# Optimization experiments

Hardware: AMD Instinct MI355X
Metric: run time of the kernel (lower is better)

The kernel has to match this reference:

```python
import jax, jax.numpy as jnp
import numpy as np

DROP_P = 0.5
DROP_KEY = jax.random.key(42)  # fixed key: deterministic dropout mask


def setup_inputs() -> dict:
    key = jax.random.key(0)
    k1, k2, k3 = jax.random.split(key, 3)
    B, H, S, D = 2, 16, 2048, 128
    x1 = jax.random.normal(k1, (B, H, S, D), dtype=jnp.float32)
    x2 = jax.random.normal(k2, (B, H, S, D), dtype=jnp.float32)
    # broadcastable per-head divisor; offset to keep it away from zero
    x3 = jax.random.uniform(k3, (B, H, 1, 1), dtype=jnp.float32) + 1.0
    return {"x1": x1, "x2": x2, "x3": x3}


def reference(x1, x2, x3):
    # v1 = x1 @ x2^T  -> [B,H,S,S]; v2 = v1 / x3 (broadcast divisor)
    scores = jnp.einsum('bhqd,bhkd->bhqk', x1, x2) / x3
    # v3 = softmax over last dim
    probs = jax.nn.softmax(scores, axis=-1)
    # v4 = dropout(p=0.5), training=True semantics: mask and rescale by 1/(1-p)
    keep = jax.random.bernoulli(DROP_KEY, 1.0 - DROP_P, probs.shape)
    probs = jnp.where(keep, probs / (1.0 - DROP_P), 0.0)
    # v5 = v4 @ x1 (note: values are x1, not a separate V); v6 = v5 + x2 residual
    out = jnp.einsum('bhqk,bhkd->bhqd', probs, x1) + x2
    return out
```

## Files before the change

kernel.cpp:

```cpp
#include <hip/hip_runtime.h>
#include <math.h>


constexpr int Sc = 2048, Dc = 128;
constexpr int NT = 32;
constexpr int BUF = 32768;
constexpr int VREL = 16384;
constexpr int POFF = 65536;

typedef short bf16x8 __attribute__((ext_vector_type(8)));
typedef float f32x4 __attribute__((ext_vector_type(4)));
union U8 { uint4 u; bf16x8 v; };

__device__ __forceinline__ unsigned rotl(unsigned x, int r) {
  return __builtin_amdgcn_alignbit(x, x, 32 - r);
}

__device__ __forceinline__ unsigned tf_o0(unsigned x1) {
  const unsigned ks1 = 42u;
  const unsigned ks2 = 0x1BD11BDAu ^ 42u;
  unsigned x0 = 0u; x1 += ks1;
#define TFR(r) { x0 += x1; x1 = rotl(x1, r); x1 ^= x0; }
  TFR(13) TFR(15) TFR(26) TFR(6)
  x0 += ks1; x1 += ks2 + 1u;
  TFR(17) TFR(29) TFR(16) TFR(24)
  x0 += ks2; x1 += 0u + 2u;
  TFR(13) TFR(15) TFR(26) TFR(6)
  x1 += ks1 + 3u;
  TFR(17) TFR(29) TFR(16) TFR(24)
  x0 += ks1; x1 += ks2 + 4u;
  TFR(13) TFR(15) TFR(26)
  x0 += x1;
  x0 += ks2;
#undef TFR
  return x0;
}

__device__ __forceinline__ unsigned keepmask(unsigned idx) {
  return (unsigned)(((int)~tf_o0(idx)) >> 31);
}

__device__ __forceinline__ unsigned pk2rn(float a, float b) {
  return __builtin_amdgcn_perm(__float_as_uint(b) + 0x8000u,
                               __float_as_uint(a) + 0x8000u, 0x07060302u);
}

__device__ __forceinline__ unsigned hw2(unsigned ma, unsigned mb) {
  return __builtin_amdgcn_perm(mb, ma, 0x05040100u);
}

__device__ __forceinline__ void gload16(const void* g, void* l) {
  __builtin_amdgcn_global_load_lds(
      (const __attribute__((address_space(1))) void*)g,
      (__attribute__((address_space(3))) void*)l, 16, 0, 0);
}

__device__ __forceinline__ void masks8(unsigned ib, unsigned km[8]) {
#pragma unroll
  for (int h2 = 0; h2 < 4; ++h2) {
    unsigned a0 = keepmask(ib + h2 * 16 + 0), a1 = keepmask(ib + h2 * 16 + 1);
    unsigned a2 = keepmask(ib + h2 * 16 + 2), a3 = keepmask(ib + h2 * 16 + 3);
    km[h2 * 2 + 0] = hw2(a0, a1);
    km[h2 * 2 + 1] = hw2(a2, a3);
  }
}

__global__ __launch_bounds__(256)
void prepack(const float* __restrict__ x1, const float* __restrict__ x2,
             uint4* __restrict__ Kb, uint4* __restrict__ Vt) {
  __shared__ ushort Kl[32 * 136];
  __shared__ ushort Vl[32 * 136];
  const int tid = threadIdx.x;
  const size_t tile = blockIdx.x;
  const float4* ks = (const float4*)(x2 + tile * 4096);
  const float4* vs = (const float4*)(x1 + tile * 4096);
#pragma unroll
  for (int it = 0; it < 4; ++it) {
    int f = it * 256 + tid;
    int row = f >> 5, c4 = f & 31;
    float4 kv = ks[f];
    float4 vv = vs[f];
    *(uint2*)&Kl[row * 136 + c4 * 4] = uint2{pk2rn(kv.x, kv.y), pk2rn(kv.z, kv.w)};
    *(uint2*)&Vl[row * 136 + c4 * 4] = uint2{pk2rn(vv.x, vv.y), pk2rn(vv.z, vv.w)};
  }
  __syncthreads();
#pragma unroll
  for (int it = 0; it < 2; ++it) {
    int u = it * 256 + tid;
    int lane = u & 63, grp = u >> 6;
    int mt = grp >> 2, c = grp & 3, m16 = lane & 15, g = lane >> 4;
    Kb[tile * 512 + u] = *(const uint4*)&Kl[(mt * 16 + m16) * 136 + c * 32 + g * 8];
  }
#pragma unroll
  for (int it = 0; it < 2; ++it) {
    int u = it * 256 + tid;
    int lane = u & 63, dt = u >> 6, m16 = lane & 15, g = lane >> 4;
    int d = dt * 16 + m16, k0 = g * 8;
    unsigned w[4];
#pragma unroll
    for (int p = 0; p < 4; ++p) {
      unsigned lo = Vl[(k0 + 2 * p) * 136 + d];
      unsigned hi = Vl[(k0 + 2 * p + 1) * 136 + d];
      w[p] = lo | (hi << 16);
    }
    Vt[tile * 512 + u] = uint4{w[0], w[1], w[2], w[3]};
  }
}

__global__ __launch_bounds__(256, 2)
void attn7(const uint4* __restrict__ Kb, const uint4* __restrict__ Vt,
           const float* __restrict__ x1, const float* __restrict__ x2,
           const float* __restrict__ x3, float* __restrict__ out) {
  __shared__ uint4 smemv[(POFF + 8192) / 16];
  char* smem = (char*)smemv;
  float* Os = (float*)smem;

  const int tid = threadIdx.x, wave = tid >> 6, lane = tid & 63;
  const int g = lane >> 4, q = lane & 15;
  const int blk = blockIdx.x, bh = blk & 31, qt = blk >> 5;

  const float* X1 = x1 + (size_t)bh * (Sc * Dc);
  const float* X2 = x2 + (size_t)bh * (Sc * Dc);
  float* outp = out + (size_t)bh * (Sc * Dc);
  const float cl2 = (1.0f / x3[bh]) * 1.4426950408889634f;

  const int qrow = qt * 64 + wave * 16 + q;
  const unsigned row_base = (unsigned)(bh * Sc + qrow) * (unsigned)Sc;
  char* prow = smem + POFF + wave * 2048 + q * 128;

  const size_t tg = (size_t)bh * 64;
  const int off = wave * 1024 + lane * 16;

  auto issue = [&](int tt, int bb) {
    const char* kg = (const char*)(Kb + (tg + 2 * tt) * 512);
    const char* vg = (const char*)(Vt + (tg + 2 * tt) * 512);
#pragma unroll
    for (int h = 0; h < 2; ++h) {
      gload16(kg + h * 8192 + off,        smem + bb + h * 8192 + off);
      gload16(kg + h * 8192 + off + 4096, smem + bb + h * 8192 + off + 4096);
      gload16(vg + h * 8192 + off,        smem + bb + VREL + h * 8192 + off);
      gload16(vg + h * 8192 + off + 4096, smem + bb + VREL + h * 8192 + off + 4096);
    }
  };

  bf16x8 qf[4];
  {
    const float4* qsrc = (const float4*)(X1 + (size_t)qrow * Dc);
#pragma unroll
    for (int c = 0; c < 4; ++c) {
      float4 f0 = qsrc[c * 8 + g * 2], f1 = qsrc[c * 8 + g * 2 + 1];
      U8 cv; cv.u = uint4{pk2rn(f0.x, f0.y), pk2rn(f0.z, f0.w),
                          pk2rn(f1.x, f1.y), pk2rn(f1.z, f1.w)};
      qf[c] = cv.v;
    }
  }

  f32x4 o[8];
#pragma unroll
  for (int i = 0; i < 8; ++i) o[i] = f32x4{0.f, 0.f, 0.f, 0.f};
  float l_run = 0.0f;

  issue(0, 0);
  __builtin_amdgcn_sched_barrier(0);
  unsigned kmc[8], kmn[8];
  masks8(row_base + (unsigned)(g * 4), kmc);

  for (int t = 0; t < NT; ++t) {
    __syncthreads();

    if (t < NT - 1) issue(t + 1, ((t + 1) & 1) * BUF);
    __builtin_amdgcn_sched_barrier(0);

    const char* kb = smem + (t & 1) * BUF;
    const char* vb = kb + VREL;

    f32x4 s0 = {}, s1 = {}, s2 = {}, s3 = {};
#pragma unroll
    for (int c = 0; c < 4; ++c) {
      U8 a0; a0.u = *(const uint4*)(kb +        ((0 * 4 + c) * 64 + lane) * 16);
      U8 a1; a1.u = *(const uint4*)(kb +        ((1 * 4 + c) * 64 + lane) * 16);
      U8 a2; a2.u = *(const uint4*)(kb + 8192 + ((0 * 4 + c) * 64 + lane) * 16);
      U8 a3; a3.u = *(const uint4*)(kb + 8192 + ((1 * 4 + c) * 64 + lane) * 16);
      s0 = __builtin_amdgcn_mfma_f32_16x16x32_bf16(a0.v, qf[c], s0, 0, 0, 0);
      s1 = __builtin_amdgcn_mfma_f32_16x16x32_bf16(a1.v, qf[c], s1, 0, 0, 0);
      s2 = __builtin_amdgcn_mfma_f32_16x16x32_bf16(a2.v, qf[c], s2, 0, 0, 0);
      s3 = __builtin_amdgcn_mfma_f32_16x16x32_bf16(a3.v, qf[c], s3, 0, 0, 0);
    }

    if (t < NT - 1)
      masks8(row_base + (unsigned)((t + 1) * 64) + (unsigned)(g * 4), kmn);

    float pr[16];
    float ls = 0.0f;
#pragma unroll
    for (int i = 0; i < 4; ++i) { pr[i]      = __builtin_amdgcn_exp2f(s0[i] * cl2); ls += pr[i]; }
#pragma unroll
    for (int i = 0; i < 4; ++i) { pr[4 + i]  = __builtin_amdgcn_exp2f(s1[i] * cl2); ls += pr[4 + i]; }
#pragma unroll
    for (int i = 0; i < 4; ++i) { pr[8 + i]  = __builtin_amdgcn_exp2f(s2[i] * cl2); ls += pr[8 + i]; }
#pragma unroll
    for (int i = 0; i < 4; ++i) { pr[12 + i] = __builtin_amdgcn_exp2f(s3[i] * cl2); ls += pr[12 + i]; }
    ls += __shfl_xor(ls, 16);
    ls += __shfl_xor(ls, 32);
    l_run += ls;

#pragma unroll
    for (int h2 = 0; h2 < 4; ++h2) {
      unsigned w0 = pk2rn(pr[h2 * 4 + 0], pr[h2 * 4 + 1]) & kmc[h2 * 2 + 0];
      unsigned w1 = pk2rn(pr[h2 * 4 + 2], pr[h2 * 4 + 3]) & kmc[h2 * 2 + 1];
      int u = (h2 >> 1) * 8 + (h2 & 1) * 4 + g;
      *(uint2*)(prow + ((u ^ q) & 15) * 8) = uint2{w0, w1};
    }

    U8 bf0, bf1;
    {
      int u0 = 2 * g;
      uint2 lo0 = *(const uint2*)(prow + (((u0 + 0) ^ q) & 15) * 8);
      uint2 hi0 = *(const uint2*)(prow + (((u0 + 1) ^ q) & 15) * 8);
      bf0.u = uint4{lo0.x, lo0.y, hi0.x, hi0.y};
      int u1 = 8 + 2 * g;
      uint2 lo1 = *(const uint2*)(prow + (((u1 + 0) ^ q) & 15) * 8);
      uint2 hi1 = *(const uint2*)(prow + (((u1 + 1) ^ q) & 15) * 8);
      bf1.u = uint4{lo1.x, lo1.y, hi1.x, hi1.y};
    }

#pragma unroll
    for (int dt = 0; dt < 8; ++dt) {
      U8 av0; av0.u = *(const uint4*)(vb +        (dt * 64 + lane) * 16);
      U8 av1; av1.u = *(const uint4*)(vb + 8192 + (dt * 64 + lane) * 16);
      o[dt] = __builtin_amdgcn_mfma_f32_16x16x32_bf16(av0.v, bf0.v, o[dt], 0, 0, 0);
      o[dt] = __builtin_amdgcn_mfma_f32_16x16x32_bf16(av1.v, bf1.v, o[dt], 0, 0, 0);
    }

#pragma unroll
    for (int i = 0; i < 8; ++i) kmc[i] = kmn[i];
  }

  const float invl = 2.0f / l_run;
  __syncthreads();
  {
    float* ow = Os + (size_t)(wave * 16 + q) * 132;
#pragma unroll
    for (int dt = 0; dt < 8; ++dt) {
      int d = dt * 16 + g * 4;
      *(float4*)&ow[d] = float4{o[dt][0] * invl, o[dt][1] * invl,
                                o[dt][2] * invl, o[dt][3] * invl};
    }
  }
  __syncthreads();
#pragma unroll
  for (int it = 0; it < 8; ++it) {
    int f = it * 256 + tid;
    int ql = f >> 5, c4 = f & 31;
    float4 ov = *(const float4*)&Os[ql * 132 + c4 * 4];
    size_t goff = (size_t)(qt * 64 + ql) * Dc + c4 * 4;
    float4 xv = *(const float4*)&X2[goff];
    *(float4*)&outp[goff] = float4{ov.x + xv.x, ov.y + xv.y, ov.z + xv.z, ov.w + xv.w};
  }
}

extern "C" void kernel_launch(void* const* d_in, const int* in_sizes, int n_in,
                              void* d_out, int out_size, void* d_ws, size_t ws_size,
                              hipStream_t stream) {
  const float* x1 = (const float*)d_in[0];
  const float* x2 = (const float*)d_in[1];
  const float* x3 = (const float*)d_in[2];
  float* out = (float*)d_out;
  const size_t PREP = (size_t)2048 * 512 * 16;
  uint4* Kb = (uint4*)d_ws;
  uint4* Vtg = (uint4*)((char*)d_ws + PREP);
  prepack<<<2048, 256, 0, stream>>>(x1, x2, Kb, Vtg);
  attn7<<<1024, 256, 0, stream>>>(Kb, Vtg, x1, x2, x3, out);
}
```

Measured before the change: 402.5 us.

## Precompute dropout keep-mask bits in prepack and stream them into attention

The Threefry-based dropout mask is now computed once per element in the prepack kernel and packed as 16-bit words in the workspace, laid out in the attention kernel's per-thread access order. The attention kernel then loads one 16-bit mask word per tile per thread, prefetched one tile ahead, instead of hashing 16 indices inline. This takes the integer hash work out of the MFMA/exp loop. In exchange, prepack does all the hashing serially per thread and writes a 16 MB mask buffer that attention must read back.

Result: no change. 410.2 us (+1.9%).

```diff
diff --git a/kernel.cpp b/kernel.cpp
--- a/kernel.cpp
+++ b/kernel.cpp
@@ -36,8 +36,8 @@
   return x0;
 }
 
-__device__ __forceinline__ unsigned keepmask(unsigned idx) {
-  return (unsigned)(((int)~tf_o0(idx)) >> 31);
+__device__ __forceinline__ unsigned kb(unsigned mw, int pos) {
+  return (unsigned)(((int)(mw << (31 - pos))) >> 31);
 }
 
 __device__ __forceinline__ unsigned pk2rn(float a, float b) {
@@ -55,21 +55,13 @@
       (__attribute__((address_space(3))) void*)l, 16, 0, 0);
 }
 
-__device__ __forceinline__ void masks8(unsigned ib, unsigned km[8]) {
-#pragma unroll
-  for (int h2 = 0; h2 < 4; ++h2) {
-    unsigned a0 = keepmask(ib + h2 * 16 + 0), a1 = keepmask(ib + h2 * 16 + 1);
-    unsigned a2 = keepmask(ib + h2 * 16 + 2), a3 = keepmask(ib + h2 * 16 + 3);
-    km[h2 * 2 + 0] = hw2(a0, a1);
-    km[h2 * 2 + 1] = hw2(a2, a3);
-  }
-}
-
 __global__ __launch_bounds__(256)
 void prepack(const float* __restrict__ x1, const float* __restrict__ x2,
-             uint4* __restrict__ Kb, uint4* __restrict__ Vt) {
+             uint4* __restrict__ Kb, uint4* __restrict__ Vt,
+             unsigned* __restrict__ Mw) {
   __shared__ ushort Kl[32 * 136];
   __shared__ ushort Vl[32 * 136];
+  __shared__ ushort Ml[32 * 128];
   const int tid = threadIdx.x;
   const size_t tile = blockIdx.x;
   const float4* ks = (const float4*)(x2 + tile * 4096);
@@ -83,7 +75,31 @@
     *(uint2*)&Kl[row * 136 + c4 * 4] = uint2{pk2rn(kv.x, kv.y), pk2rn(kv.z, kv.w)};
     *(uint2*)&Vl[row * 136 + c4 * 4] = uint2{pk2rn(vv.x, vv.y), pk2rn(vv.z, vv.w)};
   }
+
+  {
+    const unsigned a    = (unsigned)tile * 128u + (unsigned)(tid >> 1);
+    const unsigned th   = (unsigned)(tid & 1);
+    const unsigned ablk = a >> 8, atid = a & 255u;
+    const unsigned bh = ablk & 31u, qt = ablk >> 5;
+    const unsigned wv = atid >> 6, ln = atid & 63u;
+    const unsigned g = ln >> 4, q = ln & 15u;
+    const unsigned row = bh * 2048u + qt * 64u + wv * 16u + q;
+    const unsigned fb = row * 2048u + g * 4u + th * 1024u;
+    const int atid2 = tid >> 1;
+    for (int tt = 0; tt < 16; ++tt) {
+      unsigned w = 0;
+#pragma unroll
+      for (int h2 = 0; h2 < 4; ++h2)
+#pragma unroll
+        for (int i = 0; i < 4; ++i) {
+          unsigned o0 = tf_o0(fb + (unsigned)(tt * 64 + h2 * 16 + i));
+          w |= (o0 >> 31) << (h2 * 4 + i);
+        }
+      Ml[(th * 16 + tt) * 128 + atid2] = (ushort)(~w & 0xFFFFu);
+    }
+  }
   __syncthreads();
+
 #pragma unroll
   for (int it = 0; it < 2; ++it) {
     int u = it * 256 + tid;
@@ -105,10 +121,22 @@
     }
     Vt[tile * 512 + u] = uint4{w[0], w[1], w[2], w[3]};
   }
+
+  {
+    const unsigned ablk = (unsigned)(tile >> 1), h = (unsigned)(tile & 1);
+    const unsigned* Mu = (const unsigned*)Ml;
+#pragma unroll
+    for (int k = 0; k < 8; ++k) {
+      int L = tid + k * 256;
+      int t = L >> 6, j2 = L & 63;
+      Mw[ablk * 4096u + (unsigned)t * 128u + h * 64u + (unsigned)j2] = Mu[L];
+    }
+  }
 }
 
 __global__ __launch_bounds__(256, 2)
-void attn7(const uint4* __restrict__ Kb, const uint4* __restrict__ Vt,
+void attn8(const uint4* __restrict__ Kb, const uint4* __restrict__ Vt,
+           const ushort* __restrict__ Mwu,
            const float* __restrict__ x1, const float* __restrict__ x2,
            const float* __restrict__ x3, float* __restrict__ out) {
   __shared__ uint4 smemv[(POFF + 8192) / 16];
@@ -125,11 +153,11 @@
   const float cl2 = (1.0f / x3[bh]) * 1.4426950408889634f;
 
   const int qrow = qt * 64 + wave * 16 + q;
-  const unsigned row_base = (unsigned)(bh * Sc + qrow) * (unsigned)Sc;
   char* prow = smem + POFF + wave * 2048 + q * 128;
 
   const size_t tg = (size_t)bh * 64;
   const int off = wave * 1024 + lane * 16;
+  const unsigned mbase = (unsigned)blk * 8192u + (unsigned)tid;
 
   auto issue = [&](int tt, int bb) {
     const char* kg = (const char*)(Kb + (tg + 2 * tt) * 512);
@@ -162,34 +190,34 @@
 
   issue(0, 0);
   __builtin_amdgcn_sched_barrier(0);
-  unsigned kmc[8], kmn[8];
-  masks8(row_base + (unsigned)(g * 4), kmc);
+  unsigned mwc = Mwu[mbase];
+  unsigned mwn = 0;
 
   for (int t = 0; t < NT; ++t) {
     __syncthreads();
 
-    if (t < NT - 1) issue(t + 1, ((t + 1) & 1) * BUF);
+    if (t < NT - 1) {
+      issue(t + 1, ((t + 1) & 1) * BUF);
+      mwn = Mwu[mbase + (unsigned)(t + 1) * 256u];
+    }
     __builtin_amdgcn_sched_barrier(0);
 
-    const char* kb = smem + (t & 1) * BUF;
-    const char* vb = kb + VREL;
+    const char* kb_ = smem + (t & 1) * BUF;
+    const char* vb = kb_ + VREL;
 
     f32x4 s0 = {}, s1 = {}, s2 = {}, s3 = {};
 #pragma unroll
     for (int c = 0; c < 4; ++c) {
-      U8 a0; a0.u = *(const uint4*)(kb +        ((0 * 4 + c) * 64 + lane) * 16);
-      U8 a1; a1.u = *(const uint4*)(kb +        ((1 * 4 + c) * 64 + lane) * 16);
-      U8 a2; a2.u = *(const uint4*)(kb + 8192 + ((0 * 4 + c) * 64 + lane) * 16);
-      U8 a3; a3.u = *(const uint4*)(kb + 8192 + ((1 * 4 + c) * 64 + lane) * 16);
+      U8 a0; a0.u = *(const uint4*)(kb_ +        ((0 * 4 + c) * 64 + lane) * 16);
+      U8 a1; a1.u = *(const uint4*)(kb_ +        ((1 * 4 + c) * 64 + lane) * 16);
+      U8 a2; a2.u = *(const uint4*)(kb_ + 8192 + ((0 * 4 + c) * 64 + lane) * 16);
+      U8 a3; a3.u = *(const uint4*)(kb_ + 8192 + ((1 * 4 + c) * 64 + lane) * 16);
       s0 = __builtin_amdgcn_mfma_f32_16x16x32_bf16(a0.v, qf[c], s0, 0, 0, 0);
       s1 = __builtin_amdgcn_mfma_f32_16x16x32_bf16(a1.v, qf[c], s1, 0, 0, 0);
       s2 = __builtin_amdgcn_mfma_f32_16x16x32_bf16(a2.v, qf[c], s2, 0, 0, 0);
       s3 = __builtin_amdgcn_mfma_f32_16x16x32_bf16(a3.v, qf[c], s3, 0, 0, 0);
     }
 
-    if (t < NT - 1)
-      masks8(row_base + (unsigned)((t + 1) * 64) + (unsigned)(g * 4), kmn);
-
     float pr[16];
     float ls = 0.0f;
 #pragma unroll
@@ -206,8 +234,10 @@
 
 #pragma unroll
     for (int h2 = 0; h2 < 4; ++h2) {
-      unsigned w0 = pk2rn(pr[h2 * 4 + 0], pr[h2 * 4 + 1]) & kmc[h2 * 2 + 0];
-      unsigned w1 = pk2rn(pr[h2 * 4 + 2], pr[h2 * 4 + 3]) & kmc[h2 * 2 + 1];
+      unsigned m0 = hw2(kb(mwc, h2 * 4 + 0), kb(mwc, h2 * 4 + 1));
+      unsigned m1 = hw2(kb(mwc, h2 * 4 + 2), kb(mwc, h2 * 4 + 3));
+      unsigned w0 = pk2rn(pr[h2 * 4 + 0], pr[h2 * 4 + 1]) & m0;
+      unsigned w1 = pk2rn(pr[h2 * 4 + 2], pr[h2 * 4 + 3]) & m1;
       int u = (h2 >> 1) * 8 + (h2 & 1) * 4 + g;
       *(uint2*)(prow + ((u ^ q) & 15) * 8) = uint2{w0, w1};
     }
@@ -232,8 +262,7 @@
       o[dt] = __builtin_amdgcn_mfma_f32_16x16x32_bf16(av1.v, bf1.v, o[dt], 0, 0, 0);
     }
 
-#pragma unroll
-    for (int i = 0; i < 8; ++i) kmc[i] = kmn[i];
+    mwc = mwn;
   }
 
   const float invl = 2.0f / l_run;
@@ -269,6 +298,7 @@
   const size_t PREP = (size_t)2048 * 512 * 16;
   uint4* Kb = (uint4*)d_ws;
   uint4* Vtg = (uint4*)((char*)d_ws + PREP);
-  prepack<<<2048, 256, 0, stream>>>(x1, x2, Kb, Vtg);
-  attn7<<<1024, 256, 0, stream>>>(Kb, Vtg, x1, x2, x3, out);
-}
+  unsigned* Mw = (unsigned*)((char*)d_ws + 2 * PREP);
+  prepack<<<2048, 256, 0, stream>>>(x1, x2, Kb, Vtg, Mw);
+  attn8<<<1024, 256, 0, stream>>>(Kb, Vtg, (const ushort*)Mw, x1, x2, x3, out);
+}
```

## Load K/V tiles directly from global into registers, drop LDS double buffering

Applied to the files above, without the earlier changes.

Replaces the async global-to-LDS double-buffered K/V staging with per-wave direct global loads into registers, since each wave reads the full K/V tile anyway (served from L2). LDS usage shrinks to the small P-transpose scratch and launch bounds rise to 8 blocks per SM for more occupancy. The epilogue now writes output directly from registers instead of staging through LDS. It risks exposed global-load latency without explicit prefetch, redundant L2 traffic across the four waves, and register pressure limiting the intended occupancy.

Result: slower. 892.2 us (+121.7%).

```diff
diff --git a/kernel.cpp b/kernel.cpp
--- a/kernel.cpp
+++ b/kernel.cpp
@@ -4,9 +4,6 @@
 
 constexpr int Sc = 2048, Dc = 128;
 constexpr int NT = 32;
-constexpr int BUF = 32768;
-constexpr int VREL = 16384;
-constexpr int POFF = 65536;
 
 typedef short bf16x8 __attribute__((ext_vector_type(8)));
 typedef float f32x4 __attribute__((ext_vector_type(4)));
@@ -49,12 +46,6 @@
   return __builtin_amdgcn_perm(mb, ma, 0x05040100u);
 }
 
-__device__ __forceinline__ void gload16(const void* g, void* l) {
-  __builtin_amdgcn_global_load_lds(
-      (const __attribute__((address_space(1))) void*)g,
-      (__attribute__((address_space(3))) void*)l, 16, 0, 0);
-}
-
 __device__ __forceinline__ void masks8(unsigned ib, unsigned km[8]) {
 #pragma unroll
   for (int h2 = 0; h2 < 4; ++h2) {
@@ -107,13 +98,12 @@
   }
 }
 
-__global__ __launch_bounds__(256, 2)
-void attn7(const uint4* __restrict__ Kb, const uint4* __restrict__ Vt,
-           const float* __restrict__ x1, const float* __restrict__ x2,
-           const float* __restrict__ x3, float* __restrict__ out) {
-  __shared__ uint4 smemv[(POFF + 8192) / 16];
+__global__ __launch_bounds__(256, 8)
+void attn11(const uint4* __restrict__ Kb, const uint4* __restrict__ Vt,
+            const float* __restrict__ x1, const float* __restrict__ x2,
+            const float* __restrict__ x3, float* __restrict__ out) {
+  __shared__ uint4 smemv[8192 / 16];
   char* smem = (char*)smemv;
-  float* Os = (float*)smem;
 
   const int tid = threadIdx.x, wave = tid >> 6, lane = tid & 63;
   const int g = lane >> 4, q = lane & 15;
@@ -126,22 +116,9 @@
 
   const int qrow = qt * 64 + wave * 16 + q;
   const unsigned row_base = (unsigned)(bh * Sc + qrow) * (unsigned)Sc;
-  char* prow = smem + POFF + wave * 2048 + q * 128;
+  char* prow = smem + wave * 2048 + q * 128;
 
   const size_t tg = (size_t)bh * 64;
-  const int off = wave * 1024 + lane * 16;
-
-  auto issue = [&](int tt, int bb) {
-    const char* kg = (const char*)(Kb + (tg + 2 * tt) * 512);
-    const char* vg = (const char*)(Vt + (tg + 2 * tt) * 512);
-#pragma unroll
-    for (int h = 0; h < 2; ++h) {
-      gload16(kg + h * 8192 + off,        smem + bb + h * 8192 + off);
-      gload16(kg + h * 8192 + off + 4096, smem + bb + h * 8192 + off + 4096);
-      gload16(vg + h * 8192 + off,        smem + bb + VREL + h * 8192 + off);
-      gload16(vg + h * 8192 + off + 4096, smem + bb + VREL + h * 8192 + off + 4096);
-    }
-  };
 
   bf16x8 qf[4];
   {
@@ -160,35 +137,34 @@
   for (int i = 0; i < 8; ++i) o[i] = f32x4{0.f, 0.f, 0.f, 0.f};
   float l_run = 0.0f;
 
-  issue(0, 0);
-  __builtin_amdgcn_sched_barrier(0);
-  unsigned kmc[8], kmn[8];
-  masks8(row_base + (unsigned)(g * 4), kmc);
-
   for (int t = 0; t < NT; ++t) {
-    __syncthreads();
-
-    if (t < NT - 1) issue(t + 1, ((t + 1) & 1) * BUF);
-    __builtin_amdgcn_sched_barrier(0);
-
-    const char* kb = smem + (t & 1) * BUF;
-    const char* vb = kb + VREL;
+    const uint4* Kg = Kb + (tg + 2 * (size_t)t) * 512;
+    const uint4* Vg = Vt + (tg + 2 * (size_t)t) * 512;
+
+    U8 kf[16];
+#pragma unroll
+    for (int mc = 0; mc < 8; ++mc) kf[mc].u      = Kg[mc * 64 + lane];
+#pragma unroll
+    for (int mc = 0; mc < 8; ++mc) kf[8 + mc].u  = Kg[512 + mc * 64 + lane];
+
+    unsigned km[8];
+    masks8(row_base + (unsigned)(t * 64) + (unsigned)(g * 4), km);
 
     f32x4 s0 = {}, s1 = {}, s2 = {}, s3 = {};
 #pragma unroll
     for (int c = 0; c < 4; ++c) {
-      U8 a0; a0.u = *(const uint4*)(kb +        ((0 * 4 + c) * 64 + lane) * 16);
-      U8 a1; a1.u = *(const uint4*)(kb +        ((1 * 4 + c) * 64 + lane) * 16);
-      U8 a2; a2.u = *(const uint4*)(kb + 8192 + ((0 * 4 + c) * 64 + lane) * 16);
-      U8 a3; a3.u = *(const uint4*)(kb + 8192 + ((1 * 4 + c) * 64 + lane) * 16);
-      s0 = __builtin_amdgcn_mfma_f32_16x16x32_bf16(a0.v, qf[c], s0, 0, 0, 0);
-      s1 = __builtin_amdgcn_mfma_f32_16x16x32_bf16(a1.v, qf[c], s1, 0, 0, 0);
-      s2 = __builtin_amdgcn_mfma_f32_16x16x32_bf16(a2.v, qf[c], s2, 0, 0, 0);
-      s3 = __builtin_amdgcn_mfma_f32_16x16x32_bf16(a3.v, qf[c], s3, 0, 0, 0);
-    }
-
-    if (t < NT - 1)
-      masks8(row_base + (unsigned)((t + 1) * 64) + (unsigned)(g * 4), kmn);
+      s0 = __builtin_amdgcn_mfma_f32_16x16x32_bf16(kf[c].v,      qf[c], s0, 0, 0, 0);
+      s1 = __builtin_amdgcn_mfma_f32_16x16x32_bf16(kf[4 + c].v,  qf[c], s1, 0, 0, 0);
+      s2 = __builtin_amdgcn_mfma_f32_16x16x32_bf16(kf[8 + c].v,  qf[c], s2, 0, 0, 0);
+      s3 = __builtin_amdgcn_mfma_f32_16x16x32_bf16(kf[12 + c].v, qf[c], s3, 0, 0, 0);
+    }
+
+    U8 vf0[8], vf1[8];
+#pragma unroll
+    for (int dt = 0; dt < 8; ++dt) {
+      vf0[dt].u = Vg[dt * 64 + lane];
+      vf1[dt].u = Vg[512 + dt * 64 + lane];
+    }
 
     float pr[16];
     float ls = 0.0f;
@@ -206,8 +182,8 @@
 
 #pragma unroll
     for (int h2 = 0; h2 < 4; ++h2) {
-      unsigned w0 = pk2rn(pr[h2 * 4 + 0], pr[h2 * 4 + 1]) & kmc[h2 * 2 + 0];
-      unsigned w1 = pk2rn(pr[h2 * 4 + 2], pr[h2 * 4 + 3]) & kmc[h2 * 2 + 1];
+      unsigned w0 = pk2rn(pr[h2 * 4 + 0], pr[h2 * 4 + 1]) & km[h2 * 2 + 0];
+      unsigned w1 = pk2rn(pr[h2 * 4 + 2], pr[h2 * 4 + 3]) & km[h2 * 2 + 1];
       int u = (h2 >> 1) * 8 + (h2 & 1) * 4 + g;
       *(uint2*)(prow + ((u ^ q) & 15) * 8) = uint2{w0, w1};
     }
@@ -226,36 +202,20 @@
 
 #pragma unroll
     for (int dt = 0; dt < 8; ++dt) {
-      U8 av0; av0.u = *(const uint4*)(vb +        (dt * 64 + lane) * 16);
-      U8 av1; av1.u = *(const uint4*)(vb + 8192 + (dt * 64 + lane) * 16);
-      o[dt] = __builtin_amdgcn_mfma_f32_16x16x32_bf16(av0.v, bf0.v, o[dt], 0, 0, 0);
-      o[dt] = __builtin_amdgcn_mfma_f32_16x16x32_bf16(av1.v, bf1.v, o[dt], 0, 0, 0);
-    }
-
-#pragma unroll
-    for (int i = 0; i < 8; ++i) kmc[i] = kmn[i];
+      o[dt] = __builtin_amdgcn_mfma_f32_16x16x32_bf16(vf0[dt].v, bf0.v, o[dt], 0, 0, 0);
+      o[dt] = __builtin_amdgcn_mfma_f32_16x16x32_bf16(vf1[dt].v, bf1.v, o[dt], 0, 0, 0);
+    }
   }
 
   const float invl = 2.0f / l_run;
-  __syncthreads();
-  {
-    float* ow = Os + (size_t)(wave * 16 + q) * 132;
-#pragma unroll
-    for (int dt = 0; dt < 8; ++dt) {
-      int d = dt * 16 + g * 4;
-      *(float4*)&ow[d] = float4{o[dt][0] * invl, o[dt][1] * invl,
-                                o[dt][2] * invl, o[dt][3] * invl};
-    }
-  }
-  __syncthreads();
-#pragma unroll
-  for (int it = 0; it < 8; ++it) {
-    int f = it * 256 + tid;
-    int ql = f >> 5, c4 = f & 31;
-    float4 ov = *(const float4*)&Os[ql * 132 + c4 * 4];
-    size_t goff = (size_t)(qt * 64 + ql) * Dc + c4 * 4;
-    float4 xv = *(const float4*)&X2[goff];
-    *(float4*)&outp[goff] = float4{ov.x + xv.x, ov.y + xv.y, ov.z + xv.z, ov.w + xv.w};
+  const float* X2r = X2 + (size_t)qrow * Dc;
+  float* outr = outp + (size_t)qrow * Dc;
+#pragma unroll
+  for (int dt = 0; dt < 8; ++dt) {
+    int d = dt * 16 + g * 4;
+    float4 xv = *(const float4*)&X2r[d];
+    *(float4*)&outr[d] = float4{o[dt][0] * invl + xv.x, o[dt][1] * invl + xv.y,
+                                o[dt][2] * invl + xv.z, o[dt][3] * invl + xv.w};
   }
 }
 
@@ -270,5 +230,5 @@
   uint4* Kb = (uint4*)d_ws;
   uint4* Vtg = (uint4*)((char*)d_ws + PREP);
   prepack<<<2048, 256, 0, stream>>>(x1, x2, Kb, Vtg);
-  attn7<<<1024, 256, 0, stream>>>(Kb, Vtg, x1, x2, x3, out);
-}
+  attn11<<<1024, 256, 0, stream>>>(Kb, Vtg, x1, x2, x3, out);
+}
```
